# Performance work log

Measured on AMD Instinct MI355X. Metric: run time of the kernel, lower is better.

The kernel has to match this reference:

```python
import jax, jax.numpy as jnp
import numpy as np

N = 100000      # nodes
E = 1600000     # edges
NFEAT = 256
NHID = 128
NCLASS = 41


def setup_inputs() -> dict:
    key = jax.random.key(0)
    ks = jax.random.split(key, 6)
    x = jax.random.normal(ks[0], (N, NFEAT), dtype=jnp.float32)
    edge_index = jax.random.randint(ks[1], (2, E), 0, N, dtype=jnp.int32)
    edge_weight = jax.random.uniform(ks[2], (E,), dtype=jnp.float32)
    # GCNConv glorot-initialized weights + zero bias
    s1 = float(np.sqrt(6.0 / (NFEAT + NHID)))
    s2 = float(np.sqrt(6.0 / (NHID + NCLASS)))
    W1 = jax.random.uniform(ks[3], (NFEAT, NHID), jnp.float32, -s1, s1)
    b1 = jnp.zeros((NHID,), jnp.float32)
    W2 = jax.random.uniform(ks[4], (NHID, NCLASS), jnp.float32, -s2, s2)
    b2 = jnp.zeros((NCLASS,), jnp.float32)
    return {"x": x, "edge_index": edge_index, "edge_weight": edge_weight,
            "W1": W1, "b1": b1, "W2": W2, "b2": b2}


def reference(x, edge_index, edge_weight, W1, b1, W2, b2):
    # --- gcn_norm: add self-loops (weight 1), symmetric degree normalization ---
    loop = jnp.arange(N, dtype=edge_index.dtype)
    src = jnp.concatenate([edge_index[0], loop])          # [E+N]
    dst = jnp.concatenate([edge_index[1], loop])          # [E+N]
    w = jnp.concatenate([edge_weight, jnp.ones((N,), edge_weight.dtype)])
    deg = jax.ops.segment_sum(w, dst, num_segments=N)     # [N]
    dinv = jnp.where(deg > 0, jax.lax.rsqrt(deg), 0.0)
    norm = dinv[src] * w * dinv[dst]                      # [E+N]

    def gcn_conv(h, W, b):
        h = jnp.dot(h, W)                                 # [N, out]
        msg = norm[:, None] * h[src]                      # gather + scale
        return jax.ops.segment_sum(msg, dst, num_segments=N) + b

    h = jax.nn.relu(gcn_conv(x, W1, b1))
    # dropout is identity in eval mode
    out = gcn_conv(h, W2, b2)
    return jax.nn.log_softmax(out, axis=1)
```

## Files before the change

### kernel.cpp

```cpp
#include <hip/hip_runtime.h>

#define NNODES 100000
#define NEDGES 1600000
#define NFEAT  256
#define NHID   128
#define NCLASS 41
#define H2S    48
#define SCAN_B 256
#define NB1    ((NNODES + SCAN_B - 1) / SCAN_B)

typedef __attribute__((ext_vector_type(8))) short bf16x8;
typedef __attribute__((ext_vector_type(4))) float f32x4;
typedef __attribute__((ext_vector_type(4))) unsigned short us4;
typedef unsigned short u16;
typedef unsigned int u32;
typedef unsigned long long u64;

__device__ __forceinline__ float bf2f(u32 bits16) {
    union { u32 i; float f; } v; v.i = bits16 << 16; return v.f;
}
__device__ __forceinline__ u16 f2bf(float f) {
    union { u32 i; float f; } v; v.f = f;
    return (u16)((v.i + 0x7fff + ((v.i >> 16) & 1)) >> 16);
}
__device__ __forceinline__ void gload_lds16(const u16* g, u16* l) {
    __builtin_amdgcn_global_load_lds((const __attribute__((address_space(1))) u32*)g,
                                     (__attribute__((address_space(3))) u32*)l, 16, 0, 0);
}

__global__ __launch_bounds__(256) void k_hist(const int* __restrict__ dst, const float* __restrict__ w,
                                              u64* __restrict__ hist, u16* __restrict__ rank) {
    int e = blockIdx.x * 256 + threadIdx.x;
    if (e < NEDGES) {
        u64 pack = ((u64)1 << 48) + (u64)(w[e] * 4294967296.0f);
        u64 old = atomicAdd(&hist[dst[e]], pack);
        rank[e] = (u16)(old >> 48);
    }
}

__global__ __launch_bounds__(SCAN_B) void k_scan1(const u64* __restrict__ hist, const float* __restrict__ W1,
                                                  u16* __restrict__ W1t, float* __restrict__ dinv,
                                                  int* __restrict__ incl, int* __restrict__ bsum) {
    __shared__ int sm[SCAN_B];
    int i = blockIdx.x * SCAN_B + threadIdx.x;
    int v = 0;
    if (i < NNODES) {
        u64 p = hist[i];
        v = (int)(p >> 48);
        dinv[i] = rsqrtf((float)(p & 0xFFFFFFFFFFFFULL) * (1.0f / 4294967296.0f) + 1.0f);
    }
    if (i < NFEAT * NHID) {
        int k = i >> 7, n = i & 127;
        W1t[n * NFEAT + k] = f2bf(W1[i]);
    }
    sm[threadIdx.x] = v;
    __syncthreads();
    for (int o = 1; o < SCAN_B; o <<= 1) {
        int t = (threadIdx.x >= (unsigned)o) ? sm[threadIdx.x - o] : 0;
        __syncthreads();
        sm[threadIdx.x] += t;
        __syncthreads();
    }
    if (i < NNODES) incl[i] = sm[threadIdx.x];
    if (threadIdx.x == SCAN_B - 1) bsum[blockIdx.x] = sm[threadIdx.x];
}

__global__ __launch_bounds__(512) void k_scan2(int* __restrict__ bsum) {
    __shared__ int sm[512];
    int tid = threadIdx.x;
    int v = (tid < NB1) ? bsum[tid] : 0;
    sm[tid] = v;
    __syncthreads();
    for (int o = 1; o < 512; o <<= 1) {
        int t = (tid >= o) ? sm[tid - o] : 0;
        __syncthreads();
        sm[tid] += t;
        __syncthreads();
    }
    if (tid < NB1) bsum[tid] = sm[tid] - v;
}

__global__ __launch_bounds__(256) void k_scan3(const int* __restrict__ incl, const u64* __restrict__ hist,
                                               const int* __restrict__ boff, int* __restrict__ rowptr) {
    int i = blockIdx.x * 256 + threadIdx.x;
    if (i < NNODES) {
        int cntv = (int)(hist[i] >> 48);
        int ex = incl[i] - cntv + boff[i >> 8];
        rowptr[i] = ex;
        if (i == NNODES - 1) rowptr[NNODES] = ex + cntv;
    }
}

__global__ __launch_bounds__(256) void k_scatter(const int* __restrict__ src, const int* __restrict__ dst,
                                                 const float* __restrict__ w, const float* __restrict__ dinv,
                                                 const int* __restrict__ rowptr, const u16* __restrict__ rank,
                                                 uint2* __restrict__ ecsr) {
    int e = blockIdx.x * 256 + threadIdx.x;
    if (e < NEDGES) {
        int s = src[e], d = dst[e];
        int pos = rowptr[d] + (int)rank[e];
        float nv = dinv[s] * w[e] * dinv[d];
        ecsr[pos] = make_uint2((u32)s, __float_as_uint(nv));
    }
}

__global__ __launch_bounds__(256) void k_gemm1(const float* __restrict__ x, const u16* __restrict__ W1t,
                                               u16* __restrict__ h1) {
    __shared__ u16 Asm[2][8192];
    __shared__ u16 Bsm[2][8192];
    const int tid  = threadIdx.x;
    const int lane = tid & 63;
    const int w    = tid >> 6;
    const int wm   = w >> 1, wn = w & 1;
    const int row16 = lane & 15, g = lane >> 4;
    const int m0   = blockIdx.x * 128;
    const int swz  = (row16 & 7) << 3;

    f32x4 acc[4][4];
#pragma unroll
    for (int i = 0; i < 4; ++i)
#pragma unroll
        for (int j = 0; j < 4; ++j) acc[i][j] = (f32x4){0.f, 0.f, 0.f, 0.f};

    float4 areg[8];

    auto loadA = [&](int k0) {
#pragma unroll
        for (int i = 0; i < 8; ++i) {
            int s = tid + i * 256;
            int row = s >> 4, c4 = s & 15;
            int gr = m0 + row;
            if (gr < NNODES) areg[i] = *(const float4*)(x + (size_t)gr * NFEAT + k0 + c4 * 4);
            else             areg[i] = make_float4(0.f, 0.f, 0.f, 0.f);
        }
    };
    auto writeA = [&](int buf) {
#pragma unroll
        for (int i = 0; i < 8; ++i) {
            int s = tid + i * 256;
            int row = s >> 4, c4 = s & 15;
            int idx = row * 64 + ((c4 * 4) ^ ((row & 7) << 3));
            us4 h;
            h.x = f2bf(areg[i].x); h.y = f2bf(areg[i].y);
            h.z = f2bf(areg[i].z); h.w = f2bf(areg[i].w);
            *(us4*)(&Asm[buf][idx]) = h;
        }
    };
    auto stageB = [&](int buf, int k0) {
#pragma unroll
        for (int it = 0; it < 4; ++it) {
            int lin = w * 2048 + it * 512;
            int n_l = (lin + lane * 8) >> 6;
            int c_l = lane & 7;
            int gofs = n_l * NFEAT + k0 + ((c_l ^ (n_l & 7)) << 3);
            gload_lds16(W1t + gofs, &Bsm[buf][lin]);
        }
    };
    auto compute = [&](int buf) {
#pragma unroll
        for (int kk2 = 0; kk2 < 2; ++kk2) {
            bf16x8 af[4], bfr[4];
#pragma unroll
            for (int f = 0; f < 4; ++f) {
                int m_l = wm * 64 + f * 16 + row16;
                af[f]  = *(const bf16x8*)(&Asm[buf][m_l * 64 + ((kk2 * 32 + g * 8) ^ swz)]);
                int n_l = wn * 64 + f * 16 + row16;
                bfr[f] = *(const bf16x8*)(&Bsm[buf][n_l * 64 + ((kk2 * 32 + g * 8) ^ swz)]);
            }
#pragma unroll
            for (int fm = 0; fm < 4; ++fm)
#pragma unroll
                for (int fn = 0; fn < 4; ++fn)
                    acc[fm][fn] = __builtin_amdgcn_mfma_f32_16x16x32_bf16(af[fm], bfr[fn], acc[fm][fn], 0, 0, 0);
        }
    };

    loadA(0);
    stageB(0, 0);
    writeA(0);
    __syncthreads();
    int buf = 0;
    for (int step = 0; step < 4; ++step) {
        if (step < 3) { loadA((step + 1) * 64); stageB(buf ^ 1, (step + 1) * 64); }
        compute(buf);
        if (step < 3) writeA(buf ^ 1);
        __syncthreads();
        buf ^= 1;
    }

#pragma unroll
    for (int fm = 0; fm < 4; ++fm) {
        int mg = m0 + wm * 64 + fm * 16 + g * 4;
#pragma unroll
        for (int r = 0; r < 4; ++r) {
            int m_glob = mg + r;
            if (m_glob < NNODES) {
                size_t base = (size_t)m_glob * NHID + wn * 64 + row16;
#pragma unroll
                for (int fn = 0; fn < 4; ++fn)
                    h1[base + fn * 16] = f2bf(acc[fm][fn][r]);
            }
        }
    }
}

__global__ __launch_bounds__(256) void k_agg1_csr(const int* __restrict__ rowptr, const uint2* __restrict__ ecsr,
                                                  const u16* __restrict__ h1, const float* __restrict__ dinv,
                                                  const float* __restrict__ b1, u16* __restrict__ a1) {
    int node = (blockIdx.x * 256 + threadIdx.x) >> 6;
    int lane = threadIdx.x & 63;
    if (node >= NNODES) return;
    int beg = rowptr[node], end = rowptr[node + 1];
    float acc0 = 0.f, acc1 = 0.f;
    int j = beg;
    for (; j + 3 < end; j += 4) {
        uint2 e0 = ecsr[j], e1 = ecsr[j + 1], e2 = ecsr[j + 2], e3 = ecsr[j + 3];
        u32 u0 = *(const u32*)(h1 + (size_t)e0.x * NHID + lane * 2);
        u32 u1 = *(const u32*)(h1 + (size_t)e1.x * NHID + lane * 2);
        u32 u2 = *(const u32*)(h1 + (size_t)e2.x * NHID + lane * 2);
        u32 u3 = *(const u32*)(h1 + (size_t)e3.x * NHID + lane * 2);
        float n0 = __uint_as_float(e0.y), n1 = __uint_as_float(e1.y);
        float n2 = __uint_as_float(e2.y), n3 = __uint_as_float(e3.y);
        acc0 += n0 * bf2f(u0 & 0xffff) + n1 * bf2f(u1 & 0xffff)
              + n2 * bf2f(u2 & 0xffff) + n3 * bf2f(u3 & 0xffff);
        acc1 += n0 * bf2f(u0 >> 16) + n1 * bf2f(u1 >> 16)
              + n2 * bf2f(u2 >> 16) + n3 * bf2f(u3 >> 16);
    }
    for (; j < end; ++j) {
        uint2 e = ecsr[j];
        float nv = __uint_as_float(e.y);
        u32 u = *(const u32*)(h1 + (size_t)e.x * NHID + lane * 2);
        acc0 += nv * bf2f(u & 0xffff);
        acc1 += nv * bf2f(u >> 16);
    }
    float sl = dinv[node];
    sl = sl * sl;
    u32 us = *(const u32*)(h1 + (size_t)node * NHID + lane * 2);
    float2 bb = *(const float2*)(b1 + lane * 2);
    float r0 = fmaxf(acc0 + sl * bf2f(us & 0xffff) + bb.x, 0.f);
    float r1 = fmaxf(acc1 + sl * bf2f(us >> 16)    + bb.y, 0.f);
    u32 o = (u32)f2bf(r0) | ((u32)f2bf(r1) << 16);
    *(u32*)(a1 + (size_t)node * NHID + lane * 2) = o;
}

__global__ __launch_bounds__(256) void k_gemm2(const u16* __restrict__ a1, const float* __restrict__ W2,
                                               u16* __restrict__ h2p) {
    int row = blockIdx.x * 256 + threadIdx.x;
    if (row >= NNODES) return;
    float acc[NCLASS];
#pragma unroll
    for (int c = 0; c < NCLASS; ++c) acc[c] = 0.f;
    const u16* ar = a1 + (size_t)row * NHID;
    for (int k = 0; k < NHID; k += 4) {
        uint2 u = *(const uint2*)(ar + k);
        float x0 = bf2f(u.x & 0xffff), x1 = bf2f(u.x >> 16);
        float x2 = bf2f(u.y & 0xffff), x3 = bf2f(u.y >> 16);
        const float* w0 = W2 + k * NCLASS;
#pragma unroll
        for (int c = 0; c < NCLASS; ++c)
            acc[c] += x0 * w0[c] + x1 * w0[NCLASS + c] + x2 * w0[2 * NCLASS + c] + x3 * w0[3 * NCLASS + c];
    }
    u32* o = (u32*)(h2p + (size_t)row * H2S);
#pragma unroll
    for (int c = 0; c < 20; ++c)
        o[c] = (u32)f2bf(acc[2 * c]) | ((u32)f2bf(acc[2 * c + 1]) << 16);
    h2p[(size_t)row * H2S + 40] = f2bf(acc[40]);
}

__global__ __launch_bounds__(256) void k_agg2_csr(const int* __restrict__ rowptr, const uint2* __restrict__ ecsr,
                                                  const u16* __restrict__ h2p, const float* __restrict__ dinv,
                                                  const float* __restrict__ b2, float* __restrict__ out) {
    int node = (blockIdx.x * 256 + threadIdx.x) >> 6;
    int lane = threadIdx.x & 63;
    if (node >= NNODES) return;
    int beg = rowptr[node], end = rowptr[node + 1];
    float acc = 0.f;
    int j = beg;
    for (; j + 3 < end; j += 4) {
        uint2 e0 = ecsr[j], e1 = ecsr[j + 1], e2 = ecsr[j + 2], e3 = ecsr[j + 3];
        if (lane < NCLASS) {
            float h0 = bf2f(h2p[(size_t)e0.x * H2S + lane]);
            float h1v = bf2f(h2p[(size_t)e1.x * H2S + lane]);
            float h2v = bf2f(h2p[(size_t)e2.x * H2S + lane]);
            float h3 = bf2f(h2p[(size_t)e3.x * H2S + lane]);
            acc += __uint_as_float(e0.y) * h0 + __uint_as_float(e1.y) * h1v
                 + __uint_as_float(e2.y) * h2v + __uint_as_float(e3.y) * h3;
        }
    }
    for (; j < end; ++j) {
        uint2 e = ecsr[j];
        if (lane < NCLASS) acc += __uint_as_float(e.y) * bf2f(h2p[(size_t)e.x * H2S + lane]);
    }
    float sl = dinv[node];
    sl = sl * sl;
    float v = -1e30f;
    if (lane < NCLASS) v = acc + sl * bf2f(h2p[(size_t)node * H2S + lane]) + b2[lane];
    float m = v;
#pragma unroll
    for (int o = 32; o >= 1; o >>= 1) m = fmaxf(m, __shfl_xor(m, o));
    float ex = (lane < NCLASS) ? expf(v - m) : 0.f;
    float s_ = ex;
#pragma unroll
    for (int o = 32; o >= 1; o >>= 1) s_ += __shfl_xor(s_, o);
    float ls = logf(s_) + m;
    if (lane < NCLASS) out[(size_t)node * NCLASS + lane] = v - ls;
}

extern "C" void kernel_launch(void* const* d_in, const int* in_sizes, int n_in,
                              void* d_out, int out_size, void* d_ws, size_t ws_size,
                              hipStream_t stream) {
    const float* x  = (const float*)d_in[0];
    const int*   ei = (const int*)d_in[1];
    const float* ew = (const float*)d_in[2];
    const float* W1 = (const float*)d_in[3];
    const float* b1 = (const float*)d_in[4];
    const float* W2 = (const float*)d_in[5];
    const float* b2 = (const float*)d_in[6];
    float* out = (float*)d_out;
    const int* srcp = ei;
    const int* dstp = ei + NEDGES;

    char* ws = (char*)d_ws;
    auto take = [&](size_t bytes) {
        char* p = ws;
        ws += (bytes + 255) & ~(size_t)255;
        return p;
    };
    u64*   hist   = (u64*)take((size_t)NNODES * 8);
    u16*   rank   = (u16*)take((size_t)NEDGES * 2);
    float* dinv   = (float*)take((size_t)NNODES * 4);
    int*   incl   = (int*)take((size_t)NNODES * 4);
    int*   bsum   = (int*)take((size_t)NB1 * 4);
    int*   rowptr = (int*)take((size_t)(NNODES + 1) * 4);
    uint2* ecsr   = (uint2*)take((size_t)NEDGES * 8);
    u16*   W1t    = (u16*)take((size_t)NFEAT * NHID * 2);
    u16*   h1     = (u16*)take((size_t)NNODES * NHID * 2);
    u16*   a1     = (u16*)take((size_t)NNODES * NHID * 2);
    u16*   h2p    = (u16*)take((size_t)NNODES * H2S * 2);

    hipMemsetAsync(hist, 0, (size_t)NNODES * 8, stream);

    k_hist<<<(NEDGES + 255) / 256, 256, 0, stream>>>(dstp, ew, hist, rank);
    k_scan1<<<NB1, SCAN_B, 0, stream>>>(hist, W1, W1t, dinv, incl, bsum);
    k_scan2<<<1, 512, 0, stream>>>(bsum);
    k_scan3<<<(NNODES + 255) / 256, 256, 0, stream>>>(incl, hist, bsum, rowptr);
    k_scatter<<<(NEDGES + 255) / 256, 256, 0, stream>>>(srcp, dstp, ew, dinv, rowptr, rank, ecsr);
    k_gemm1<<<(NNODES + 127) / 128, 256, 0, stream>>>(x, W1t, h1);
    k_agg1_csr<<<(NNODES * 64 + 255) / 256, 256, 0, stream>>>(rowptr, ecsr, h1, dinv, b1, a1);
    k_gemm2<<<(NNODES + 255) / 256, 256, 0, stream>>>(a1, W2, h2p);
    k_agg2_csr<<<(NNODES * 64 + 255) / 256, 256, 0, stream>>>(rowptr, ecsr, h2p, dinv, b2, out);
}
```

Baseline: 524.6 us.

## Pre-convert x to bf16 in hist kernel, stage via direct LDS loads; pack agg2 two nodes per wave

x is converted to bf16 inside the edge histogram kernel, so gemm1 can stage A tiles with direct global-to-LDS loads, the same way it already stages W1t, instead of loading fp32 into registers and converting. The bf16 copy of x shares one workspace region with a1 and h2p, padded to 100096 rows so the unguarded A loads in the last tile stay in bounds. The second-layer aggregation now packs two nodes per 64-lane wave and reads two classes per lane as 32-bit words. This cuts idle lanes and gather instructions. In exchange, x is written and read one extra time, as a half-size bf16 copy.

```diff
diff --git a/kernel.cpp b/kernel.cpp
--- a/kernel.cpp
+++ b/kernel.cpp
@@ -8,10 +8,11 @@
 #define H2S    48
 #define SCAN_B 256
 #define NB1    ((NNODES + SCAN_B - 1) / SCAN_B)
+#define XROWS  100096
 
 typedef __attribute__((ext_vector_type(8))) short bf16x8;
 typedef __attribute__((ext_vector_type(4))) float f32x4;
-typedef __attribute__((ext_vector_type(4))) unsigned short us4;
+typedef __attribute__((ext_vector_type(8))) unsigned short us8;
 typedef unsigned short u16;
 typedef unsigned int u32;
 typedef unsigned long long u64;
@@ -29,12 +30,26 @@
 }
 
 __global__ __launch_bounds__(256) void k_hist(const int* __restrict__ dst, const float* __restrict__ w,
-                                              u64* __restrict__ hist, u16* __restrict__ rank) {
+                                              u64* __restrict__ hist, u16* __restrict__ rank,
+                                              const float* __restrict__ x, u16* __restrict__ xb) {
     int e = blockIdx.x * 256 + threadIdx.x;
     if (e < NEDGES) {
         u64 pack = ((u64)1 << 48) + (u64)(w[e] * 4294967296.0f);
         u64 old = atomicAdd(&hist[dst[e]], pack);
         rank[e] = (u16)(old >> 48);
+    }
+    size_t base = (size_t)e * 16;
+    if (base < (size_t)NNODES * NFEAT) {
+        float4 v0 = *(const float4*)(x + base);
+        float4 v1 = *(const float4*)(x + base + 4);
+        float4 v2 = *(const float4*)(x + base + 8);
+        float4 v3 = *(const float4*)(x + base + 12);
+        us8 h0 = {f2bf(v0.x), f2bf(v0.y), f2bf(v0.z), f2bf(v0.w),
+                  f2bf(v1.x), f2bf(v1.y), f2bf(v1.z), f2bf(v1.w)};
+        us8 h1 = {f2bf(v2.x), f2bf(v2.y), f2bf(v2.z), f2bf(v2.w),
+                  f2bf(v3.x), f2bf(v3.y), f2bf(v3.z), f2bf(v3.w)};
+        *(us8*)(xb + base)     = h0;
+        *(us8*)(xb + base + 8) = h1;
     }
 }
 
@@ -104,7 +119,7 @@
     }
 }
 
-__global__ __launch_bounds__(256) void k_gemm1(const float* __restrict__ x, const u16* __restrict__ W1t,
+__global__ __launch_bounds__(256) void k_gemm1(const u16* __restrict__ xb, const u16* __restrict__ W1t,
                                                u16* __restrict__ h1) {
     __shared__ u16 Asm[2][8192];
     __shared__ u16 Bsm[2][8192];
@@ -122,28 +137,14 @@
 #pragma unroll
         for (int j = 0; j < 4; ++j) acc[i][j] = (f32x4){0.f, 0.f, 0.f, 0.f};
 
-    float4 areg[8];
-
-    auto loadA = [&](int k0) {
-#pragma unroll
-        for (int i = 0; i < 8; ++i) {
-            int s = tid + i * 256;
-            int row = s >> 4, c4 = s & 15;
-            int gr = m0 + row;
-            if (gr < NNODES) areg[i] = *(const float4*)(x + (size_t)gr * NFEAT + k0 + c4 * 4);
-            else             areg[i] = make_float4(0.f, 0.f, 0.f, 0.f);
-        }
-    };
-    auto writeA = [&](int buf) {
-#pragma unroll
-        for (int i = 0; i < 8; ++i) {
-            int s = tid + i * 256;
-            int row = s >> 4, c4 = s & 15;
-            int idx = row * 64 + ((c4 * 4) ^ ((row & 7) << 3));
-            us4 h;
-            h.x = f2bf(areg[i].x); h.y = f2bf(areg[i].y);
-            h.z = f2bf(areg[i].z); h.w = f2bf(areg[i].w);
-            *(us4*)(&Asm[buf][idx]) = h;
+    auto stageA = [&](int buf, int k0) {
+#pragma unroll
+        for (int it = 0; it < 4; ++it) {
+            int lin = w * 2048 + it * 512;
+            int row = (lin + lane * 8) >> 6;
+            int c_l = lane & 7;
+            int gofs = (m0 + row) * NFEAT + k0 + ((c_l ^ (row & 7)) << 3);
+            gload_lds16(xb + gofs, &Asm[buf][lin]);
         }
     };
     auto stageB = [&](int buf, int k0) {
@@ -175,15 +176,13 @@
         }
     };
 
-    loadA(0);
+    stageA(0, 0);
     stageB(0, 0);
-    writeA(0);
     __syncthreads();
     int buf = 0;
     for (int step = 0; step < 4; ++step) {
-        if (step < 3) { loadA((step + 1) * 64); stageB(buf ^ 1, (step + 1) * 64); }
+        if (step < 3) { stageA(buf ^ 1, (step + 1) * 64); stageB(buf ^ 1, (step + 1) * 64); }
         compute(buf);
-        if (step < 3) writeA(buf ^ 1);
         __syncthreads();
         buf ^= 1;
     }
@@ -264,46 +263,62 @@
 #pragma unroll
     for (int c = 0; c < 20; ++c)
         o[c] = (u32)f2bf(acc[2 * c]) | ((u32)f2bf(acc[2 * c + 1]) << 16);
-    h2p[(size_t)row * H2S + 40] = f2bf(acc[40]);
+    o[20] = (u32)f2bf(acc[40]);
 }
 
 __global__ __launch_bounds__(256) void k_agg2_csr(const int* __restrict__ rowptr, const uint2* __restrict__ ecsr,
-                                                  const u16* __restrict__ h2p, const float* __restrict__ dinv,
+                                                  const u32* __restrict__ h2p32, const float* __restrict__ dinv,
                                                   const float* __restrict__ b2, float* __restrict__ out) {
-    int node = (blockIdx.x * 256 + threadIdx.x) >> 6;
-    int lane = threadIdx.x & 63;
+    int wid  = (blockIdx.x * 256 + threadIdx.x) >> 6;
+    int node = wid * 2 + ((threadIdx.x >> 5) & 1);
+    int l    = threadIdx.x & 31;
     if (node >= NNODES) return;
+    int c0 = l * 2, c1 = c0 + 1;
+    bool ok0 = (c0 < NCLASS), ok1 = (c1 < NCLASS);
     int beg = rowptr[node], end = rowptr[node + 1];
-    float acc = 0.f;
+    float acc0 = 0.f, acc1 = 0.f;
     int j = beg;
     for (; j + 3 < end; j += 4) {
         uint2 e0 = ecsr[j], e1 = ecsr[j + 1], e2 = ecsr[j + 2], e3 = ecsr[j + 3];
-        if (lane < NCLASS) {
-            float h0 = bf2f(h2p[(size_t)e0.x * H2S + lane]);
-            float h1v = bf2f(h2p[(size_t)e1.x * H2S + lane]);
-            float h2v = bf2f(h2p[(size_t)e2.x * H2S + lane]);
-            float h3 = bf2f(h2p[(size_t)e3.x * H2S + lane]);
-            acc += __uint_as_float(e0.y) * h0 + __uint_as_float(e1.y) * h1v
-                 + __uint_as_float(e2.y) * h2v + __uint_as_float(e3.y) * h3;
+        if (ok0) {
+            u32 u0 = h2p32[(size_t)e0.x * 24 + l];
+            u32 u1 = h2p32[(size_t)e1.x * 24 + l];
+            u32 u2 = h2p32[(size_t)e2.x * 24 + l];
+            u32 u3 = h2p32[(size_t)e3.x * 24 + l];
+            float n0 = __uint_as_float(e0.y), n1 = __uint_as_float(e1.y);
+            float n2 = __uint_as_float(e2.y), n3 = __uint_as_float(e3.y);
+            acc0 += n0 * bf2f(u0 & 0xffff) + n1 * bf2f(u1 & 0xffff)
+                  + n2 * bf2f(u2 & 0xffff) + n3 * bf2f(u3 & 0xffff);
+            acc1 += n0 * bf2f(u0 >> 16) + n1 * bf2f(u1 >> 16)
+                  + n2 * bf2f(u2 >> 16) + n3 * bf2f(u3 >> 16);
         }
     }
     for (; j < end; ++j) {
         uint2 e = ecsr[j];
-        if (lane < NCLASS) acc += __uint_as_float(e.y) * bf2f(h2p[(size_t)e.x * H2S + lane]);
+        if (ok0) {
+            u32 u = h2p32[(size_t)e.x * 24 + l];
+            float nv = __uint_as_float(e.y);
+            acc0 += nv * bf2f(u & 0xffff);
+            acc1 += nv * bf2f(u >> 16);
+        }
     }
     float sl = dinv[node];
     sl = sl * sl;
-    float v = -1e30f;
-    if (lane < NCLASS) v = acc + sl * bf2f(h2p[(size_t)node * H2S + lane]) + b2[lane];
-    float m = v;
-#pragma unroll
-    for (int o = 32; o >= 1; o >>= 1) m = fmaxf(m, __shfl_xor(m, o));
-    float ex = (lane < NCLASS) ? expf(v - m) : 0.f;
-    float s_ = ex;
-#pragma unroll
-    for (int o = 32; o >= 1; o >>= 1) s_ += __shfl_xor(s_, o);
-    float ls = logf(s_) + m;
-    if (lane < NCLASS) out[(size_t)node * NCLASS + lane] = v - ls;
+    float v0 = -1e30f, v1 = -1e30f;
+    if (ok0) {
+        u32 u = h2p32[(size_t)node * 24 + l];
+        v0 = acc0 + sl * bf2f(u & 0xffff) + b2[c0];
+        if (ok1) v1 = acc1 + sl * bf2f(u >> 16) + b2[c1];
+    }
+    float m = fmaxf(v0, v1);
+#pragma unroll
+    for (int o = 16; o >= 1; o >>= 1) m = fmaxf(m, __shfl_xor(m, o, 32));
+    float ex = (ok0 ? expf(v0 - m) : 0.f) + (ok1 ? expf(v1 - m) : 0.f);
+#pragma unroll
+    for (int o = 16; o >= 1; o >>= 1) ex += __shfl_xor(ex, o, 32);
+    float ls = logf(ex) + m;
+    if (ok0) out[(size_t)node * NCLASS + c0] = v0 - ls;
+    if (ok1) out[(size_t)node * NCLASS + c1] = v1 - ls;
 }
 
 extern "C" void kernel_launch(void* const* d_in, const int* in_sizes, int n_in,
@@ -335,18 +350,22 @@
     uint2* ecsr   = (uint2*)take((size_t)NEDGES * 8);
     u16*   W1t    = (u16*)take((size_t)NFEAT * NHID * 2);
     u16*   h1     = (u16*)take((size_t)NNODES * NHID * 2);
-    u16*   a1     = (u16*)take((size_t)NNODES * NHID * 2);
-    u16*   h2p    = (u16*)take((size_t)NNODES * H2S * 2);
+    size_t xb_bytes  = (size_t)XROWS * NFEAT * 2;
+    size_t a1_bytes  = (size_t)NNODES * NHID * 2;
+    char*  region    = take(xb_bytes);
+    u16*   xb  = (u16*)region;
+    u16*   a1  = (u16*)region;
+    u16*   h2p = (u16*)(region + a1_bytes);
 
     hipMemsetAsync(hist, 0, (size_t)NNODES * 8, stream);
 
-    k_hist<<<(NEDGES + 255) / 256, 256, 0, stream>>>(dstp, ew, hist, rank);
+    k_hist<<<(NEDGES + 255) / 256, 256, 0, stream>>>(dstp, ew, hist, rank, x, xb);
     k_scan1<<<NB1, SCAN_B, 0, stream>>>(hist, W1, W1t, dinv, incl, bsum);
     k_scan2<<<1, 512, 0, stream>>>(bsum);
     k_scan3<<<(NNODES + 255) / 256, 256, 0, stream>>>(incl, hist, bsum, rowptr);
     k_scatter<<<(NEDGES + 255) / 256, 256, 0, stream>>>(srcp, dstp, ew, dinv, rowptr, rank, ecsr);
-    k_gemm1<<<(NNODES + 127) / 128, 256, 0, stream>>>(x, W1t, h1);
+    k_gemm1<<<(NNODES + 127) / 128, 256, 0, stream>>>(xb, W1t, h1);
     k_agg1_csr<<<(NNODES * 64 + 255) / 256, 256, 0, stream>>>(rowptr, ecsr, h1, dinv, b1, a1);
     k_gemm2<<<(NNODES + 255) / 256, 256, 0, stream>>>(a1, W2, h2p);
-    k_agg2_csr<<<(NNODES * 64 + 255) / 256, 256, 0, stream>>>(rowptr, ecsr, h2p, dinv, b2, out);
-}
+    k_agg2_csr<<<(NNODES / 2 * 64 + 255) / 256, 256, 0, stream>>>(rowptr, ecsr, (const u32*)h2p, dinv, b2, out);
+}
```

After: 478.6 us. 8.8% less time.
